# Kernel tuning notes

Hardware: AMD Instinct MI355X
Metric: run time of the kernel (lower is better)

Reference implementation:

```python
import jax, jax.numpy as jnp
import numpy as np
from jax import lax

V = 100000       # vocab_size / num_words
E = 300          # embedding_size (== num_units, required by compare stage)
M = 300          # num_units / mem_dim
NC = 3           # num_classes
L = 128          # leaves per tree -> N = 2L-1 nodes
N = 2 * L - 1


def build_tree(num_leaves):
    # balanced binary tree, postorder node numbering (children before parent)
    left, right = [], []
    def rec(lo, hi):
        if hi - lo == 1:
            left.append(-1); right.append(-1)
            return len(left) - 1
        mid = (lo + hi) // 2
        l = rec(lo, mid)
        r = rec(mid, hi)
        left.append(l); right.append(r)
        return len(left) - 1
    rec(0, num_leaves)
    return np.asarray(left, np.int32), np.asarray(right, np.int32)


def setup_inputs() -> dict:
    key = jax.random.key(0)
    ks = jax.random.split(key, 20)
    l1, r1 = build_tree(L)
    l2, r2 = build_tree(L)
    s = 0.1  # param scale (stands in for orthogonal init)
    inp = {
        "sent1": jax.random.randint(ks[0], (N,), 0, V),
        "sent2": jax.random.randint(ks[1], (N,), 0, V),
        "left1": jnp.asarray(l1), "right1": jnp.asarray(r1),
        "left2": jnp.asarray(l2), "right2": jnp.asarray(r2),
        "emb": jax.random.normal(ks[2], (V, E), jnp.float32),
        # composer x-projections, gate order: [cx, ix, fx, ox]
        "Wx_i": jax.random.normal(ks[3], (4, M, E), jnp.float32) * s,
        "bx_i": jnp.zeros((4, M), jnp.float32),
        # composer h-projections, gate order: [u, i, lf, rf, o]
        "Wl_i": jax.random.normal(ks[4], (5, M, M), jnp.float32) * s,
        "Wr_i": jax.random.normal(ks[5], (5, M, M), jnp.float32) * s,
        "Wx_c": jax.random.normal(ks[6], (4, M, M), jnp.float32) * s,
        "bx_c": jnp.zeros((4, M), jnp.float32),
        "Wl_c": jax.random.normal(ks[7], (5, M, M), jnp.float32) * s,
        "Wr_c": jax.random.normal(ks[8], (5, M, M), jnp.float32) * s,
        "Wc": jax.random.normal(ks[9], (M, 4 * M), jnp.float32) * 0.01,
        "bc": jnp.zeros((M,), jnp.float32),
        "Wa1": jax.random.normal(ks[10], (M, 4 * M), jnp.float32) * 0.01,
        "ba1": jnp.zeros((M,), jnp.float32),
        "Wa2": jax.random.normal(ks[11], (NC, M), jnp.float32) * 0.01,
        "ba2": jnp.zeros((NC,), jnp.float32),
    }
    return inp


def tree_lstm(xg, left, right, Wl, Wr):
    # xg: [N, 4, M] precomputed x-gate terms (cx, ix, fx, ox)
    # Wl/Wr: [5, M, M] hidden-state gate weights (u, i, lf, rf, o)
    n, _, m = xg.shape
    zero = jnp.zeros((m,), xg.dtype)

    def step(carry, t):
        C, H = carry
        i, l, r = t
        lc = jnp.where(l >= 0, C[jnp.maximum(l, 0)], zero)
        lh = jnp.where(l >= 0, H[jnp.maximum(l, 0)], zero)
        rc = jnp.where(r >= 0, C[jnp.maximum(r, 0)], zero)
        rh = jnp.where(r >= 0, H[jnp.maximum(r, 0)], zero)
        gl = jnp.einsum('gmd,d->gm', Wl, lh)  # [5, M]
        gr = jnp.einsum('gmd,d->gm', Wr, rh)
        x = xg[i]  # [4, M]
        u  = jnp.tanh(x[0] + gl[0] + gr[0])
        ig = jax.nn.sigmoid(x[1] + gl[1] + gr[1])
        lf = jax.nn.sigmoid(x[2] + gl[2] + gr[2])  # fx shared for both forgets (as in source)
        rf = jax.nn.sigmoid(x[2] + gl[3] + gr[3])
        c = ig * u + lf * lc + rf * rc
        o = jax.nn.sigmoid(x[3] + gl[4] + gr[4])
        h = o * jnp.tanh(c)
        return (C.at[i].set(c), H.at[i].set(h)), None

    init = (jnp.zeros((n, m), xg.dtype), jnp.zeros((n, m), xg.dtype))
    (_, H), _ = lax.scan(step, init, (jnp.arange(n), left, right))
    return H  # [N, M] all node hidden states in postorder


def reference(sent1, sent2, left1, right1, left2, right2, emb,
              Wx_i, bx_i, Wl_i, Wr_i, Wx_c, bx_c, Wl_c, Wr_c,
              Wc, bc, Wa1, ba1, Wa2, ba2):
    pad = emb.shape[0] - 1  # num_words - 1

    def encode(sent, left, right):
        # leaves embed their token; internal nodes embed PAD (PAD=True path)
        tok = jnp.where(left < 0, sent, pad)
        x = emb[tok]                                        # [N, E]
        xg = jnp.einsum('nd,gmd->ngm', x, Wx_i) + bx_i      # [N, 4, M]
        return tree_lstm(xg, left, right, Wl_i, Wr_i)

    s1 = encode(sent1, left1, right1)  # [N1, M]
    s2 = encode(sent2, left2, right2)  # [N2, M]

    raw = s1 @ s2.T                                         # [N1, N2]
    beta = jax.nn.softmax(raw, axis=1) @ s2                 # aligned to s1
    alpha = jax.nn.softmax(raw.T, axis=1) @ s1              # aligned to s2

    def compare(s, a, left, right):
        feat = jnp.concatenate([s, a, s - a, s * a], axis=-1)  # [N, 4M]
        h = jax.nn.relu(feat @ Wc.T + bc)                      # [N, M]
        xg = jnp.einsum('nd,gmd->ngm', h, Wx_c) + bx_c
        return tree_lstm(xg, left, right, Wl_c, Wr_c)

    v1 = compare(s1, beta, left1, right1)
    v2 = compare(s2, alpha, left2, right2)

    agg = jnp.concatenate([v1.mean(0), v1.max(0), v2.mean(0), v2.max(0)])  # [4M]
    hidden = jax.nn.relu(agg @ Wa1.T + ba1)
    logits = hidden @ Wa2.T + ba2
    return logits[None, :]  # [1, num_classes]
```

## Files before the change

### kernel.cpp

```cpp
#include <hip/hip_runtime.h>
#include <math.h>

#define NN 255
#define TC 510
#define HTLD 512

typedef unsigned int uint32;

__device__ __forceinline__ float sigm(float x){ return 1.f/(1.f+expf(-x)); }

__device__ __forceinline__ float aload(const float* p){ return __hip_atomic_load(p, __ATOMIC_RELAXED, __HIP_MEMORY_SCOPE_AGENT); }
__device__ __forceinline__ void astore(float* p, float v){ __hip_atomic_store(p, v, __ATOMIC_RELAXED, __HIP_MEMORY_SCOPE_AGENT); }
__device__ __forceinline__ uint32 aloadu(const uint32* p){ return __hip_atomic_load(p, __ATOMIC_RELAXED, __HIP_MEMORY_SCOPE_AGENT); }
__device__ __forceinline__ void astoreu(uint32* p, uint32 v){ __hip_atomic_store(p, v, __ATOMIC_RELAXED, __HIP_MEMORY_SCOPE_AGENT); }

__device__ __forceinline__ void leaf_gate(const float* __restrict__ xgp, int m, float& c, float& h){
  float x0 = xgp[m], x1 = xgp[300+m], x3 = xgp[900+m];
  float u = tanhf(x0), ig = sigm(x1);
  c = ig * u;
  h = sigm(x3) * tanhf(c);
}

template<int NB>
__device__ __forceinline__ void gsync(uint32* flags, uint32 phase){
  asm volatile("s_waitcnt vmcnt(0)" ::: "memory");
  __syncthreads();
  uint32* gate = flags + NB;
  if (blockIdx.x == 0){
    if (threadIdx.x < 64){
      for(;;){
        uint32 mn = phase;
        for (int i = 1 + (int)threadIdx.x; i < NB; i += 64)
          mn = min(mn, aloadu(&flags[i]));
        if (__all(mn >= phase)) break;
        __builtin_amdgcn_s_sleep(2);
      }
      if (threadIdx.x == 0) astoreu(gate, phase);
    }
  } else {
    if (threadIdx.x == 0){
      astoreu(&flags[blockIdx.x], phase);
      while (aloadu(gate) < phase) __builtin_amdgcn_s_sleep(2);
    }
  }
  __syncthreads();
}

__global__ __launch_bounds__(512) void k_setup(const int* __restrict__ l1, const int* __restrict__ r1,
                                               const int* __restrict__ l2, const int* __restrict__ r2,
                                               int4* __restrict__ lists2, int* __restrict__ cnt)
{
  __shared__ int lv[TC];
  __shared__ int cs[16];
  int t = threadIdx.x;
  if (t < TC) lv[t] = 0;
  if (t < 16) cs[t] = 0;
  __syncthreads();
  for (int it = 0; it < 12; ++it){
    int nv = 0;
    if (t < TC){
      int tr = t >= NN, i = t - tr * NN;
      const int* L = tr ? l2 : l1;
      const int* R = tr ? r2 : r1;
      int l = L[i], r = R[i];
      nv = (l < 0) ? 0 : 1 + max(lv[tr * NN + l], lv[tr * NN + r]);
    }
    __syncthreads();
    if (t < TC) lv[t] = nv;
    __syncthreads();
  }
  if (t < TC){
    int tr = t >= NN, i = t - tr * NN;
    int v = min(lv[t], 15);
    int pos = atomicAdd(&cs[v], 1);
    int l = (tr ? l2 : l1)[i], r = (tr ? r2 : r1)[i];
    lists2[v * 256 + pos] = make_int4(tr * NN + i, tr * NN + max(l, 0), tr * NN + max(r, 0), 0);
  }
  __syncthreads();
  if (t < 16) cnt[t] = cs[t];
}

template<int NB, int NG>
__global__ __launch_bounds__(256, 3) void k_tree(
    const int* __restrict__ l1, const int* __restrict__ l2,
    const float* __restrict__ Wl, const float* __restrict__ Wr,
    const float* __restrict__ xg,
    float* __restrict__ H, float* __restrict__ C, float* __restrict__ HT,
    const int4* __restrict__ lists2, const int* __restrict__ cnt,
    uint32* __restrict__ bar)
{
  __shared__ float Hs[16][2][320];
  __shared__ float Cs[16][4][2];
  __shared__ float Xs[16][4][4];
  __shared__ int4 nfo[288];
  __shared__ int lvoff[9];

  const int tid = threadIdx.x;
  const int lane = tid & 63, team = tid >> 6;
  const int mblk = blockIdx.x % 75, grp = blockIdx.x / 75;
  const int m = mblk * 4 + team;

  float wl[5][5], wr[5][5];
  #pragma unroll
  for (int g = 0; g < 5; ++g)
    #pragma unroll
    for (int j = 0; j < 5; ++j){
      int d = j * 64 + lane;
      size_t o = ((size_t)g * 300 + m) * 300 + d;
      wl[g][j] = (d < 300) ? Wl[o] : 0.f;
      wr[g][j] = (d < 300) ? Wr[o] : 0.f;
    }

  if (tid == 0){ int o = 0; for (int lv = 1; lv <= 7; ++lv){ lvoff[lv] = o; o += cnt[lv]; } }
  __syncthreads();
  for (int lv = 1; lv <= 7; ++lv)
    for (int i = tid; i < cnt[lv]; i += 256)
      nfo[lvoff[lv] + i] = lists2[lv * 256 + i];

  for (int e = blockIdx.x * 256 + tid; e < TC * 300; e += 256 * NB){
    int gi = e / 300, mm = e - gi * 300;
    int tr = gi >= NN, node = gi - tr * NN;
    if ((tr ? l2 : l1)[node] < 0){
      float c, h; leaf_gate(xg + (size_t)gi * 1200, mm, c, h);
      astore(&C[(size_t)gi * 300 + mm], c);
      astore(&H[(size_t)gi * 300 + mm], h);
      astore(&HT[(size_t)mm * HTLD + gi], h);
    }
  }
  gsync<NB>(bar, 1);

  for (int lv = 1; lv <= 7; ++lv){
    int nodes = cnt[lv];
    int npg = (nodes + NG - 1) / NG;
    int n0 = grp * npg, n1 = min(nodes, n0 + npg);
    for (int nb0 = n0; nb0 < n1; nb0 += 16){
      int nch = min(16, n1 - nb0);
      int base = lvoff[lv] + nb0;
      __syncthreads();
      #pragma unroll
      for (int p = 0; p < 2; ++p){
        int niA = team + p * 8, niB = niA + 4;
        bool vA = niA < nch, vB = niB < nch;
        int4 na = vA ? nfo[base + niA] : make_int4(0, 0, 0, 0);
        int4 nb4 = vB ? nfo[base + niB] : make_int4(0, 0, 0, 0);
        int d0 = lane, d1 = 64 + lane, d2 = 128 + lane, d3 = 192 + lane, d4 = 256 + lane;
        bool i4 = d4 < 300;
        #define LDH(ci, dd, ok) ((ok) ? aload(&H[(size_t)(ci) * 300 + (dd)]) : 0.f)
        float a0=LDH(na.y,d0,vA), a1=LDH(na.y,d1,vA), a2=LDH(na.y,d2,vA), a3=LDH(na.y,d3,vA), a4=LDH(na.y,d4,vA&&i4);
        float a5=LDH(na.z,d0,vA), a6=LDH(na.z,d1,vA), a7=LDH(na.z,d2,vA), a8=LDH(na.z,d3,vA), a9=LDH(na.z,d4,vA&&i4);
        float c0=LDH(nb4.y,d0,vB), c1=LDH(nb4.y,d1,vB), c2=LDH(nb4.y,d2,vB), c3=LDH(nb4.y,d3,vB), c4=LDH(nb4.y,d4,vB&&i4);
        float c5=LDH(nb4.z,d0,vB), c6=LDH(nb4.z,d1,vB), c7=LDH(nb4.z,d2,vB), c8=LDH(nb4.z,d3,vB), c9=LDH(nb4.z,d4,vB&&i4);
        #undef LDH
        if (vA){
          Hs[niA][0][d0]=a0; Hs[niA][0][d1]=a1; Hs[niA][0][d2]=a2; Hs[niA][0][d3]=a3; Hs[niA][0][d4]=a4;
          Hs[niA][1][d0]=a5; Hs[niA][1][d1]=a6; Hs[niA][1][d2]=a7; Hs[niA][1][d3]=a8; Hs[niA][1][d4]=a9;
        }
        if (vB){
          Hs[niB][0][d0]=c0; Hs[niB][0][d1]=c1; Hs[niB][0][d2]=c2; Hs[niB][0][d3]=c3; Hs[niB][0][d4]=c4;
          Hs[niB][1][d0]=c5; Hs[niB][1][d1]=c6; Hs[niB][1][d2]=c7; Hs[niB][1][d3]=c8; Hs[niB][1][d4]=c9;
        }
      }
      if (tid < 128){
        int ni = tid >> 3, tm = (tid >> 1) & 3, side = tid & 1;
        if (ni < nch){
          int4 nn = nfo[base + ni];
          int child = side ? nn.z : nn.y;
          Cs[ni][tm][side] = aload(&C[(size_t)child * 300 + mblk * 4 + tm]);
        }
      }
      {
        int ni = tid >> 4, tm = (tid >> 2) & 3, g = tid & 3;
        if (ni < nch){
          int4 nn = nfo[base + ni];
          Xs[ni][tm][g] = xg[(size_t)nn.x * 1200 + g * 300 + mblk * 4 + tm];
        }
      }
      __syncthreads();
      #pragma unroll 2
      for (int ni = 0; ni < nch; ++ni){
        float p0 = 0.f, p1 = 0.f, p2 = 0.f, p3 = 0.f, p4 = 0.f;
        #pragma unroll
        for (int j = 0; j < 5; ++j){
          float hl = Hs[ni][0][j * 64 + lane];
          float hr = Hs[ni][1][j * 64 + lane];
          p0 += wl[0][j] * hl + wr[0][j] * hr;
          p1 += wl[1][j] * hl + wr[1][j] * hr;
          p2 += wl[2][j] * hl + wr[2][j] * hr;
          p3 += wl[3][j] * hl + wr[3][j] * hr;
          p4 += wl[4][j] * hl + wr[4][j] * hr;
        }
        #pragma unroll
        for (int off = 32; off; off >>= 1){
          p0 += __shfl_xor(p0, off); p1 += __shfl_xor(p1, off); p2 += __shfl_xor(p2, off);
          p3 += __shfl_xor(p3, off); p4 += __shfl_xor(p4, off);
        }
        if (lane == 0){
          int4 nn = nfo[base + ni];
          int gi = nn.x;
          float lc = Cs[ni][team][0], rc = Cs[ni][team][1];
          float u  = tanhf(Xs[ni][team][0] + p0);
          float ig = sigm (Xs[ni][team][1] + p1);
          float lf = sigm (Xs[ni][team][2] + p2);
          float rf = sigm (Xs[ni][team][2] + p3);
          float o  = sigm (Xs[ni][team][3] + p4);
          float cc = ig * u + lf * lc + rf * rc;
          float hv = o * tanhf(cc);
          astore(&C[(size_t)gi * 300 + m], cc);
          astore(&H[(size_t)gi * 300 + m], hv);
          astore(&HT[(size_t)m * HTLD + gi], hv);
        }
      }
    }
    if (lv < 7) gsync<NB>(bar, 1 + lv);
  }
}

__global__ __launch_bounds__(256) void k_xg(const int* __restrict__ sent1, const int* __restrict__ sent2,
                                            const int* __restrict__ l1, const int* __restrict__ l2,
                                            const float* __restrict__ emb, int pad,
                                            const float* __restrict__ W, const float* __restrict__ bias,
                                            const float* __restrict__ hsrc, float* __restrict__ out)
{
  __shared__ float Z[8][300];
  int tx = threadIdx.x, ty = threadIdx.y;
  int t = ty * 64 + tx;
  int colbase = blockIdx.y * 8;
  for (int c = 0; c < 8; ++c){
    int gcol = colbase + c;
    if (gcol < TC){
      if (hsrc){
        for (int k = t; k < 300; k += 256) Z[c][k] = hsrc[(size_t)gcol * 300 + k];
      } else {
        int tr = gcol >= NN, node = gcol - tr * NN;
        int tok = ((tr ? l2 : l1)[node] < 0) ? (tr ? sent2 : sent1)[node] : pad;
        const float* e = emb + (size_t)tok * 300;
        for (int k = t; k < 300; k += 256) Z[c][k] = e[k];
      }
    } else {
      for (int k = t; k < 300; k += 256) Z[c][k] = 0.f;
    }
  }
  __syncthreads();
  int r = blockIdx.x * 64 + tx;
  if (r < 1200){
    float a0 = 0.f, a1 = 0.f;
    const float* wp = W + (size_t)r * 300;
    for (int k = 0; k < 300; k += 4){
      float4 wv = *(const float4*)(wp + k);
      float4 z0 = *(const float4*)(&Z[ty][k]);
      float4 z1 = *(const float4*)(&Z[ty + 4][k]);
      a0 += wv.x*z0.x + wv.y*z0.y + wv.z*z0.z + wv.w*z0.w;
      a1 += wv.x*z1.x + wv.y*z1.y + wv.z*z1.z + wv.w*z1.w;
    }
    float b = bias[r];
    int g0 = colbase + ty, g1 = colbase + ty + 4;
    if (g0 < TC) out[(size_t)g0 * 1200 + r] = a0 + b;
    if (g1 < TC) out[(size_t)g1 * 1200 + r] = a1 + b;
  }
}

__global__ __launch_bounds__(256) void k_attn2(const float* __restrict__ H, const float* __restrict__ HT,
                                               float* __restrict__ ab)
{
  __shared__ float q[4][304];
  __shared__ float S[4][256];
  __shared__ float red[256];
  __shared__ float invs[4];
  int t = threadIdx.x;
  int dir = blockIdx.x >= 64;
  int r0 = (blockIdx.x - dir * 64) * 4;
  int nr = min(4, NN - r0);
  const float* Ss = H + (dir ? (size_t)NN * 300 : 0);
  const float* So = H + (dir ? 0 : (size_t)NN * 300);
  int oppb = dir ? 0 : NN;

  for (int idx = t; idx < 4 * 304; idx += 256){
    int r = idx / 304, k = idx - r * 304;
    q[r][k] = (r < nr && k < 300) ? Ss[(size_t)(r0 + r) * 300 + k] : 0.f;
  }
  __syncthreads();

  float s0 = 0.f, s1 = 0.f, s2 = 0.f, s3 = 0.f;
  if (t < NN){
    const float* hp = HT + oppb + t;
    #pragma unroll 4
    for (int k = 0; k < 300; ++k){
      float ht = hp[(size_t)k * HTLD];
      s0 += q[0][k] * ht; s1 += q[1][k] * ht; s2 += q[2][k] * ht; s3 += q[3][k] * ht;
    }
  }
  S[0][t] = (t < NN) ? s0 : -1e30f;
  S[1][t] = (t < NN) ? s1 : -1e30f;
  S[2][t] = (t < NN) ? s2 : -1e30f;
  S[3][t] = (t < NN) ? s3 : -1e30f;
  __syncthreads();

  for (int r = 0; r < nr; ++r){
    red[t] = S[r][t];
    __syncthreads();
    for (int s = 128; s; s >>= 1){ if (t < s) red[t] = fmaxf(red[t], red[t + s]); __syncthreads(); }
    float mx = red[0];
    __syncthreads();
    float e = (t < NN) ? expf(S[r][t] - mx) : 0.f;
    S[r][t] = e;
    red[t] = e;
    __syncthreads();
    for (int s = 128; s; s >>= 1){ if (t < s) red[t] += red[t + s]; __syncthreads(); }
    if (t == 0) invs[r] = 1.f / red[0];
    __syncthreads();
  }

  float a0=0,a1=0,a2=0,a3=0, b0=0,b1=0,b2=0,b3=0;
  int m2 = t + 256;
  bool has2 = m2 < 300;
  for (int j = 0; j < NN; ++j){
    const float* sp = So + (size_t)j * 300;
    float v1 = (t < 300) ? sp[t] : 0.f;
    float v2 = has2 ? sp[m2] : 0.f;
    float p0 = S[0][j], p1 = S[1][j], p2 = S[2][j], p3 = S[3][j];
    a0 += p0 * v1; a1 += p1 * v1; a2 += p2 * v1; a3 += p3 * v1;
    b0 += p0 * v2; b1 += p1 * v2; b2 += p2 * v2; b3 += p3 * v2;
  }
  float accs1[4] = {a0, a1, a2, a3};
  float accs2[4] = {b0, b1, b2, b3};
  for (int r = 0; r < nr; ++r){
    size_t rowo = (size_t)(dir * NN + r0 + r) * 300;
    if (t < 300) ab[rowo + t] = accs1[r] * invs[r];
    if (has2)    ab[rowo + m2] = accs2[r] * invs[r];
  }
}

__global__ __launch_bounds__(256) void k_hcmp(const float* __restrict__ Henc, const float* __restrict__ ab,
                                              const float* __restrict__ Wc, const float* __restrict__ bc,
                                              float* __restrict__ hc)
{
  __shared__ float Z[8][1200];
  int tx = threadIdx.x, ty = threadIdx.y;
  int t = ty * 64 + tx;
  int colbase = blockIdx.y * 8;
  for (int c = 0; c < 8; ++c){
    int gcol = colbase + c;
    if (gcol < TC){
      const float* sp = Henc + (size_t)gcol * 300;
      const float* ap = ab + (size_t)gcol * 300;
      for (int k = t; k < 1200; k += 256){
        int sel = k >= 900 ? 3 : (k >= 600 ? 2 : (k >= 300 ? 1 : 0));
        int kk = k - sel * 300;
        float s = sp[kk], a = ap[kk];
        Z[c][k] = sel == 0 ? s : sel == 1 ? a : sel == 2 ? (s - a) : (s * a);
      }
    } else {
      for (int k = t; k < 1200; k += 256) Z[c][k] = 0.f;
    }
  }
  __syncthreads();
  int r = blockIdx.x * 64 + tx;
  if (r < 300){
    float a0 = 0.f, a1 = 0.f;
    const float* wp = Wc + (size_t)r * 1200;
    for (int k = 0; k < 1200; k += 4){
      float4 wv = *(const float4*)(wp + k);
      float4 z0 = *(const float4*)(&Z[ty][k]);
      float4 z1 = *(const float4*)(&Z[ty + 4][k]);
      a0 += wv.x*z0.x + wv.y*z0.y + wv.z*z0.z + wv.w*z0.w;
      a1 += wv.x*z1.x + wv.y*z1.y + wv.z*z1.z + wv.w*z1.w;
    }
    float b = bc[r];
    int g0 = colbase + ty, g1 = colbase + ty + 4;
    if (g0 < TC) hc[(size_t)g0 * 300 + r] = fmaxf(a0 + b, 0.f);
    if (g1 < TC) hc[(size_t)g1 * 300 + r] = fmaxf(a1 + b, 0.f);
  }
}

__global__ __launch_bounds__(256) void k_agg(const float* __restrict__ HTc, float* __restrict__ agg)
{
  __shared__ float red[256];
  int idx = blockIdx.x;
  int tr = idx / 300, m = idx - tr * 300;
  int t = threadIdx.x;
  const float* p = HTc + (size_t)m * HTLD + tr * NN;
  float v = (t < NN) ? p[t] : 0.f;
  red[t] = v;
  __syncthreads();
  for (int s = 128; s; s >>= 1){ if (t < s) red[t] += red[t + s]; __syncthreads(); }
  float sum = red[0];
  __syncthreads();
  red[t] = (t < NN) ? v : -1e30f;
  __syncthreads();
  for (int s = 128; s; s >>= 1){ if (t < s) red[t] = fmaxf(red[t], red[t + s]); __syncthreads(); }
  if (t == 0){
    agg[tr * 600 + m] = sum / 255.f;
    agg[tr * 600 + 300 + m] = red[0];
  }
}

__global__ __launch_bounds__(256) void k_mlp1(const float* __restrict__ agg,
                                              const float* __restrict__ Wa1, const float* __restrict__ ba1,
                                              float* __restrict__ hid)
{
  __shared__ float red[256];
  int h = blockIdx.x, t = threadIdx.x;
  const float* wp = Wa1 + (size_t)h * 1200;
  float a = 0.f;
  for (int k = t; k < 1200; k += 256) a += wp[k] * agg[k];
  red[t] = a;
  __syncthreads();
  for (int s = 128; s; s >>= 1){ if (t < s) red[t] += red[t + s]; __syncthreads(); }
  if (t == 0) hid[h] = fmaxf(red[0] + ba1[h], 0.f);
}

__global__ __launch_bounds__(256) void k_mlp2(const float* __restrict__ hid,
                                              const float* __restrict__ Wa2, const float* __restrict__ ba2,
                                              float* __restrict__ out)
{
  __shared__ float h_s[300];
  int t = threadIdx.x;
  for (int k = t; k < 300; k += 256) h_s[k] = hid[k];
  __syncthreads();
  if (t < 192){
    int c = t >> 6, ln = t & 63;
    float a = 0.f;
    for (int k = ln; k < 300; k += 64) a += Wa2[c * 300 + k] * h_s[k];
    #pragma unroll
    for (int off = 32; off; off >>= 1) a += __shfl_down(a, off);
    if (ln == 0) out[c] = a + ba2[c];
  }
}

extern "C" void kernel_launch(void* const* d_in, const int* in_sizes, int n_in,
                              void* d_out, int out_size, void* d_ws, size_t ws_size,
                              hipStream_t stream)
{
  const int*   sent1 = (const int*)d_in[0];
  const int*   sent2 = (const int*)d_in[1];
  const int*   l1    = (const int*)d_in[2];
  const int*   r1    = (const int*)d_in[3];
  const int*   l2    = (const int*)d_in[4];
  const int*   r2    = (const int*)d_in[5];
  const float* emb   = (const float*)d_in[6];
  const float* Wx_i  = (const float*)d_in[7];
  const float* bx_i  = (const float*)d_in[8];
  const float* Wl_i  = (const float*)d_in[9];
  const float* Wr_i  = (const float*)d_in[10];
  const float* Wx_c  = (const float*)d_in[11];
  const float* bx_c  = (const float*)d_in[12];
  const float* Wl_c  = (const float*)d_in[13];
  const float* Wr_c  = (const float*)d_in[14];
  const float* Wcm   = (const float*)d_in[15];
  const float* bcm   = (const float*)d_in[16];
  const float* Wa1   = (const float*)d_in[17];
  const float* ba1   = (const float*)d_in[18];
  const float* Wa2   = (const float*)d_in[19];
  const float* ba2   = (const float*)d_in[20];
  int V = in_sizes[6] / 300;
  int pad = V - 1;

  char* w = (char*)d_ws;
  uint32* bar1   = (uint32*)w;
  uint32* bar2   = (uint32*)(w + 4096);
  int*    cnt    = (int*)(w + 8192);
  int4*   lists2 = (int4*)(w + 8256);
  float* xg   = (float*)(w + 8256 + 65536);
  float* Henc = xg + 612000;
  float* Hcmp = Henc + 153000;
  float* C    = Hcmp + 153000;
  float* ab   = C + 153000;
  float* hc   = ab + 153000;
  float* HTe  = hc + 153000;
  float* HTc  = HTe + 153600;
  float* agg  = HTc + 153600;
  float* hid  = agg + 1200;
  float* outp = (float*)d_out;

  hipMemsetAsync(bar1, 0, 8192, stream);

  int nb6 = 0, nCU = 0;
  hipError_t eq = hipOccupancyMaxActiveBlocksPerMultiprocessor(&nb6, reinterpret_cast<const void*>(&k_tree<600, 8>), 256, 0);
  hipError_t ec = hipDeviceGetAttribute(&nCU, hipDeviceAttributeMultiprocessorCount, 0);
  bool ok600 = (eq == hipSuccess) && (ec == hipSuccess) && (nb6 * nCU >= 600);

  k_setup<<<1, 512, 0, stream>>>(l1, r1, l2, r2, lists2, cnt);
  dim3 blk(64, 4);

  k_xg<<<dim3(19, 64), blk, 0, stream>>>(sent1, sent2, l1, l2, emb, pad, Wx_i, bx_i, nullptr, xg);
  {
    void* args[] = {(void*)&l1, (void*)&l2, (void*)&Wl_i, (void*)&Wr_i, (void*)&xg,
                    (void*)&Henc, (void*)&C, (void*)&HTe, (void*)&lists2, (void*)&cnt, (void*)&bar1};
    if (ok600) hipLaunchCooperativeKernel((void*)&k_tree<600, 8>, dim3(600), dim3(256), args, 0, stream);
    else       hipLaunchCooperativeKernel((void*)&k_tree<300, 4>, dim3(300), dim3(256), args, 0, stream);
  }

  k_attn2<<<128, 256, 0, stream>>>(Henc, HTe, ab);

  k_hcmp<<<dim3(5, 64), blk, 0, stream>>>(Henc, ab, Wcm, bcm, hc);
  k_xg<<<dim3(19, 64), blk, 0, stream>>>(sent1, sent2, l1, l2, emb, pad, Wx_c, bx_c, hc, xg);
  {
    void* args[] = {(void*)&l1, (void*)&l2, (void*)&Wl_c, (void*)&Wr_c, (void*)&xg,
                    (void*)&Hcmp, (void*)&C, (void*)&HTc, (void*)&lists2, (void*)&cnt, (void*)&bar2};
    if (ok600) hipLaunchCooperativeKernel((void*)&k_tree<600, 8>, dim3(600), dim3(256), args, 0, stream);
    else       hipLaunchCooperativeKernel((void*)&k_tree<300, 4>, dim3(300), dim3(256), args, 0, stream);
  }

  k_agg<<<600, 256, 0, stream>>>(HTc, agg);
  k_mlp1<<<300, 256, 0, stream>>>(agg, Wa1, ba1, hid);
  k_mlp2<<<1, 256, 0, stream>>>(hid, Wa2, ba2, outp);
}
```

Measured before the change: 471.6 us.

## Replace grid-wide level barriers with per-node readiness counters in tree kernel

Removes the centralized grid barrier between tree levels and instead has each block bump a per-node counter once its slice of a node is written; consumers spin on the two child counters reaching 75 before loading child states. Leaf computation is also re-split so each block computes only its own m-slice of its assigned leaves, matching the dependency tracking. This lets levels overlap and avoids the master-block polling round trip, at the cost of many atomics and per-node spinning. The rdy counters must be zero at launch; the memset covers both rdy arrays.

```diff
diff --git a/kernel.cpp b/kernel.cpp
--- a/kernel.cpp
+++ b/kernel.cpp
@@ -12,38 +12,12 @@
 __device__ __forceinline__ float aload(const float* p){ return __hip_atomic_load(p, __ATOMIC_RELAXED, __HIP_MEMORY_SCOPE_AGENT); }
 __device__ __forceinline__ void astore(float* p, float v){ __hip_atomic_store(p, v, __ATOMIC_RELAXED, __HIP_MEMORY_SCOPE_AGENT); }
 __device__ __forceinline__ uint32 aloadu(const uint32* p){ return __hip_atomic_load(p, __ATOMIC_RELAXED, __HIP_MEMORY_SCOPE_AGENT); }
-__device__ __forceinline__ void astoreu(uint32* p, uint32 v){ __hip_atomic_store(p, v, __ATOMIC_RELAXED, __HIP_MEMORY_SCOPE_AGENT); }
 
 __device__ __forceinline__ void leaf_gate(const float* __restrict__ xgp, int m, float& c, float& h){
   float x0 = xgp[m], x1 = xgp[300+m], x3 = xgp[900+m];
   float u = tanhf(x0), ig = sigm(x1);
   c = ig * u;
   h = sigm(x3) * tanhf(c);
-}
-
-template<int NB>
-__device__ __forceinline__ void gsync(uint32* flags, uint32 phase){
-  asm volatile("s_waitcnt vmcnt(0)" ::: "memory");
-  __syncthreads();
-  uint32* gate = flags + NB;
-  if (blockIdx.x == 0){
-    if (threadIdx.x < 64){
-      for(;;){
-        uint32 mn = phase;
-        for (int i = 1 + (int)threadIdx.x; i < NB; i += 64)
-          mn = min(mn, aloadu(&flags[i]));
-        if (__all(mn >= phase)) break;
-        __builtin_amdgcn_s_sleep(2);
-      }
-      if (threadIdx.x == 0) astoreu(gate, phase);
-    }
-  } else {
-    if (threadIdx.x == 0){
-      astoreu(&flags[blockIdx.x], phase);
-      while (aloadu(gate) < phase) __builtin_amdgcn_s_sleep(2);
-    }
-  }
-  __syncthreads();
 }
 
 __global__ __launch_bounds__(512) void k_setup(const int* __restrict__ l1, const int* __restrict__ r1,
@@ -80,19 +54,19 @@
   if (t < 16) cnt[t] = cs[t];
 }
 
-template<int NB, int NG>
+template<int NG>
 __global__ __launch_bounds__(256, 3) void k_tree(
-    const int* __restrict__ l1, const int* __restrict__ l2,
     const float* __restrict__ Wl, const float* __restrict__ Wr,
     const float* __restrict__ xg,
     float* __restrict__ H, float* __restrict__ C, float* __restrict__ HT,
     const int4* __restrict__ lists2, const int* __restrict__ cnt,
-    uint32* __restrict__ bar)
-{
+    uint32* __restrict__ rdy)
+{
+  constexpr int NB = NG * 75;
   __shared__ float Hs[16][2][320];
   __shared__ float Cs[16][4][2];
   __shared__ float Xs[16][4][4];
-  __shared__ int4 nfo[288];
+  __shared__ int4 nfo[512];
   __shared__ int lvoff[9];
 
   const int tid = threadIdx.x;
@@ -111,23 +85,33 @@
       wr[g][j] = (d < 300) ? Wr[o] : 0.f;
     }
 
-  if (tid == 0){ int o = 0; for (int lv = 1; lv <= 7; ++lv){ lvoff[lv] = o; o += cnt[lv]; } }
-  __syncthreads();
-  for (int lv = 1; lv <= 7; ++lv)
+  if (tid == 0){ lvoff[0] = 0; for (int lv = 1; lv <= 7; ++lv) lvoff[lv] = lvoff[lv-1] + cnt[lv-1]; }
+  __syncthreads();
+  for (int lv = 0; lv <= 7; ++lv)
     for (int i = tid; i < cnt[lv]; i += 256)
       nfo[lvoff[lv] + i] = lists2[lv * 256 + i];
-
-  for (int e = blockIdx.x * 256 + tid; e < TC * 300; e += 256 * NB){
-    int gi = e / 300, mm = e - gi * 300;
-    int tr = gi >= NN, node = gi - tr * NN;
-    if ((tr ? l2 : l1)[node] < 0){
-      float c, h; leaf_gate(xg + (size_t)gi * 1200, mm, c, h);
-      astore(&C[(size_t)gi * 300 + mm], c);
-      astore(&H[(size_t)gi * 300 + mm], h);
-      astore(&HT[(size_t)mm * HTLD + gi], h);
-    }
-  }
-  gsync<NB>(bar, 1);
+  __syncthreads();
+
+  {
+    int nodes = cnt[0];
+    int npg = (nodes + NG - 1) / NG;
+    int n0 = grp * npg, n1 = min(nodes, n0 + npg);
+    for (int nb0 = n0; nb0 < n1; nb0 += 64){
+      int nch = min(64, n1 - nb0);
+      if (tid < nch * 4){
+        int ni = tid >> 2, tm = tid & 3;
+        int gi = nfo[nb0 + ni].x;
+        int mm = mblk * 4 + tm;
+        float c, h; leaf_gate(xg + (size_t)gi * 1200, mm, c, h);
+        astore(&C[(size_t)gi * 300 + mm], c);
+        astore(&H[(size_t)gi * 300 + mm], h);
+        astore(&HT[(size_t)mm * HTLD + gi], h);
+      }
+      asm volatile("s_waitcnt vmcnt(0)" ::: "memory");
+      __syncthreads();
+      if (tid < nch) atomicAdd(&rdy[nfo[nb0 + tid].x], 1u);
+    }
+  }
 
   for (int lv = 1; lv <= 7; ++lv){
     int nodes = cnt[lv];
@@ -136,6 +120,12 @@
     for (int nb0 = n0; nb0 < n1; nb0 += 16){
       int nch = min(16, n1 - nb0);
       int base = lvoff[lv] + nb0;
+      __syncthreads();
+      if (tid < nch){
+        int4 nn = nfo[base + tid];
+        while (aloadu(&rdy[nn.y]) < 75u) __builtin_amdgcn_s_sleep(8);
+        while (aloadu(&rdy[nn.z]) < 75u) __builtin_amdgcn_s_sleep(8);
+      }
       __syncthreads();
       #pragma unroll
       for (int p = 0; p < 2; ++p){
@@ -210,8 +200,10 @@
           astore(&HT[(size_t)m * HTLD + gi], hv);
         }
       }
-    }
-    if (lv < 7) gsync<NB>(bar, 1 + lv);
+      asm volatile("s_waitcnt vmcnt(0)" ::: "memory");
+      __syncthreads();
+      if (tid < nch) atomicAdd(&rdy[nfo[base + tid].x], 1u);
+    }
   }
 }
 
@@ -456,8 +448,8 @@
   int pad = V - 1;
 
   char* w = (char*)d_ws;
-  uint32* bar1   = (uint32*)w;
-  uint32* bar2   = (uint32*)(w + 4096);
+  uint32* rdy1   = (uint32*)w;
+  uint32* rdy2   = (uint32*)(w + 4096);
   int*    cnt    = (int*)(w + 8192);
   int4*   lists2 = (int4*)(w + 8256);
   float* xg   = (float*)(w + 8256 + 65536);
@@ -472,10 +464,10 @@
   float* hid  = agg + 1200;
   float* outp = (float*)d_out;
 
-  hipMemsetAsync(bar1, 0, 8192, stream);
+  hipMemsetAsync(rdy1, 0, 8192, stream);
 
   int nb6 = 0, nCU = 0;
-  hipError_t eq = hipOccupancyMaxActiveBlocksPerMultiprocessor(&nb6, reinterpret_cast<const void*>(&k_tree<600, 8>), 256, 0);
+  hipError_t eq = hipOccupancyMaxActiveBlocksPerMultiprocessor(&nb6, reinterpret_cast<const void*>(&k_tree<8>), 256, 0);
   hipError_t ec = hipDeviceGetAttribute(&nCU, hipDeviceAttributeMultiprocessorCount, 0);
   bool ok600 = (eq == hipSuccess) && (ec == hipSuccess) && (nb6 * nCU >= 600);
 
@@ -484,10 +476,10 @@
 
   k_xg<<<dim3(19, 64), blk, 0, stream>>>(sent1, sent2, l1, l2, emb, pad, Wx_i, bx_i, nullptr, xg);
   {
-    void* args[] = {(void*)&l1, (void*)&l2, (void*)&Wl_i, (void*)&Wr_i, (void*)&xg,
-                    (void*)&Henc, (void*)&C, (void*)&HTe, (void*)&lists2, (void*)&cnt, (void*)&bar1};
-    if (ok600) hipLaunchCooperativeKernel((void*)&k_tree<600, 8>, dim3(600), dim3(256), args, 0, stream);
-    else       hipLaunchCooperativeKernel((void*)&k_tree<300, 4>, dim3(300), dim3(256), args, 0, stream);
+    void* args[] = {(void*)&Wl_i, (void*)&Wr_i, (void*)&xg,
+                    (void*)&Henc, (void*)&C, (void*)&HTe, (void*)&lists2, (void*)&cnt, (void*)&rdy1};
+    if (ok600) hipLaunchCooperativeKernel((void*)&k_tree<8>, dim3(600), dim3(256), args, 0, stream);
+    else       hipLaunchCooperativeKernel((void*)&k_tree<4>, dim3(300), dim3(256), args, 0, stream);
   }
 
   k_attn2<<<128, 256, 0, stream>>>(Henc, HTe, ab);
@@ -495,10 +487,10 @@
   k_hcmp<<<dim3(5, 64), blk, 0, stream>>>(Henc, ab, Wcm, bcm, hc);
   k_xg<<<dim3(19, 64), blk, 0, stream>>>(sent1, sent2, l1, l2, emb, pad, Wx_c, bx_c, hc, xg);
   {
-    void* args[] = {(void*)&l1, (void*)&l2, (void*)&Wl_c, (void*)&Wr_c, (void*)&xg,
-                    (void*)&Hcmp, (void*)&C, (void*)&HTc, (void*)&lists2, (void*)&cnt, (void*)&bar2};
-    if (ok600) hipLaunchCooperativeKernel((void*)&k_tree<600, 8>, dim3(600), dim3(256), args, 0, stream);
-    else       hipLaunchCooperativeKernel((void*)&k_tree<300, 4>, dim3(300), dim3(256), args, 0, stream);
+    void* args[] = {(void*)&Wl_c, (void*)&Wr_c, (void*)&xg,
+                    (void*)&Hcmp, (void*)&C, (void*)&HTc, (void*)&lists2, (void*)&cnt, (void*)&rdy2};
+    if (ok600) hipLaunchCooperativeKernel((void*)&k_tree<8>, dim3(600), dim3(256), args, 0, stream);
+    else       hipLaunchCooperativeKernel((void*)&k_tree<4>, dim3(300), dim3(256), args, 0, stream);
   }
 
   k_agg<<<600, 256, 0, stream>>>(HTc, agg);
```

After: 489.4 us. +3.8%, slower.
